# Kernel optimization log

Hardware: AMD Instinct MI355X
Metric: run time of the kernel (lower is better)

The kernel has to match this reference:

```python
import jax, jax.numpy as jnp
import numpy as np

N, E, G = 50000, 1600000, 64
IN, HID, OUT = 128, 64, 64
NEG_SLOPE = 0.2


def _p(key, shape):
    return jax.random.normal(key, shape, dtype=jnp.float32) * 0.1


def setup_inputs() -> dict:
    key = jax.random.key(0)
    ks = jax.random.split(key, 24)
    inp = {
        "x": jax.random.normal(ks[0], (N, IN), dtype=jnp.float32),
        "edge_index": jax.random.randint(ks[1], (2, E), 0, N),
        "edge_attr": jax.random.uniform(ks[2], (E, 1), dtype=jnp.float32),
        "batch": jnp.sort(jax.random.randint(ks[3], (N,), 0, G)),
        # GATv2 layer 1 (in=128 -> 64, heads=1)
        "Wl1": _p(ks[4], (IN, HID)), "bl1": _p(ks[5], (HID,)),
        "Wr1": _p(ks[6], (IN, HID)), "br1": _p(ks[7], (HID,)),
        "We1": _p(ks[8], (1, HID)), "att1": _p(ks[9], (HID,)), "bias1": _p(ks[10], (HID,)),
        # GATv2 layer 2 (64 -> 64)
        "Wl2": _p(ks[11], (HID, OUT)), "bl2": _p(ks[12], (OUT,)),
        "Wr2": _p(ks[13], (HID, OUT)), "br2": _p(ks[14], (OUT,)),
        "We2": _p(ks[15], (1, OUT)), "att2": _p(ks[16], (OUT,)), "bias2": _p(ks[17], (OUT,)),
        # MLP head: fc1 (64->32), bn1 (32), fc3 (32->1)
        "W_fc1": _p(ks[18], (OUT, OUT // 2)), "b_fc1": _p(ks[19], (OUT // 2,)),
        "bn_gamma": jnp.ones((OUT // 2,), jnp.float32),
        "bn_beta": jnp.zeros((OUT // 2,), jnp.float32),
        "bn_mean": _p(ks[20], (OUT // 2,)),
        "bn_var": jax.random.uniform(ks[21], (OUT // 2,), jnp.float32, 0.5, 1.5),
        "W_fc3": _p(ks[22], (OUT // 2, 1)), "b_fc3": _p(ks[23], (1,)),
    }
    return inp


def _add_self_loops(src, dst, edge_attr, n):
    # PyG add_self_loops with fill_value='mean': loop attr = mean of incoming edge attrs per node
    s = jax.ops.segment_sum(edge_attr, dst, num_segments=n)  # (N,1)
    c = jax.ops.segment_sum(jnp.ones((edge_attr.shape[0], 1), edge_attr.dtype), dst, num_segments=n)
    loop_attr = s / jnp.maximum(c, 1.0)
    loops = jnp.arange(n)
    return (jnp.concatenate([src, loops]), jnp.concatenate([dst, loops]),
            jnp.concatenate([edge_attr, loop_attr], axis=0))


def _gatv2(h, src, dst, e_attr, Wl, bl, Wr, br, We, att, bias, n):
    xl = h @ Wl + bl                     # (N, C) source transform
    xr = h @ Wr + br                     # (N, C) target transform
    ef = e_attr @ We                     # (E', C)
    s = jax.nn.leaky_relu(xl[src] + xr[dst] + ef, NEG_SLOPE)  # (E', C)
    logits = s @ att                     # (E',)
    m = jax.ops.segment_max(logits, dst, num_segments=n)
    m = jnp.where(jnp.isfinite(m), m, 0.0)
    p = jnp.exp(logits - m[dst])
    denom = jax.ops.segment_sum(p, dst, num_segments=n)
    alpha = p / (denom[dst] + 1e-16)
    out = jax.ops.segment_sum(alpha[:, None] * xl[src], dst, num_segments=n)
    return out + bias


def reference(x, edge_index, edge_attr, batch,
              Wl1, bl1, Wr1, br1, We1, att1, bias1,
              Wl2, bl2, Wr2, br2, We2, att2, bias2,
              W_fc1, b_fc1, bn_gamma, bn_beta, bn_mean, bn_var, W_fc3, b_fc3):
    n = x.shape[0]
    src, dst, ea = _add_self_loops(edge_index[0], edge_index[1], edge_attr, n)
    h = jax.nn.elu(_gatv2(x, src, dst, ea, Wl1, bl1, Wr1, br1, We1, att1, bias1, n))
    h = jax.nn.elu(_gatv2(h, src, dst, ea, Wl2, bl2, Wr2, br2, We2, att2, bias2, n))
    # global_mean_pool
    sums = jax.ops.segment_sum(h, batch, num_segments=G)
    cnts = jax.ops.segment_sum(jnp.ones((n, 1), h.dtype), batch, num_segments=G)
    pooled = sums / jnp.maximum(cnts, 1.0)
    # head: bn1(relu(fc1(.))) with eval-mode BN, dropout off, then fc3
    z = jax.nn.relu(pooled @ W_fc1 + b_fc1)
    z = (z - bn_mean) / jnp.sqrt(bn_var + 1e-5) * bn_gamma + bn_beta
    return z @ W_fc3 + b_fc3
```

## Files before the change

kernel.cpp:

```cpp
#include <hip/hip_runtime.h>
#include <hip/hip_fp16.h>
#include <math.h>

typedef unsigned long long u64;
typedef __attribute__((ext_vector_type(2))) _Float16 half2v;
typedef __attribute__((ext_vector_type(4))) _Float16 half4v;


#define CAP     3008
#define MAXSPAN 3072
#define PEPB    4096

__device__ __forceinline__ void xf_block(
        const float* __restrict__ h, int ld,
        const float* __restrict__ Wl, const float* __restrict__ bl,
        const float* __restrict__ Wr, const float* __restrict__ br,
        __half* __restrict__ xl, __half* __restrict__ xr,
        int N, int node0, _Float16* rows, int t) {
    int in_dim = 1 << ld;
    int q = in_dim >> 2;
    for (int idx = t; idx < 64 * q; idx += 256) {
        int nn = idx >> (ld - 2);
        int kk = (idx & (q - 1)) << 2;
        int node = node0 + nn;
        float4 v = {0.f, 0.f, 0.f, 0.f};
        if (node < N) v = *(const float4*)(h + (((size_t)node) << ld) + kk);
        half4v hv = {(_Float16)v.x, (_Float16)v.y, (_Float16)v.z, (_Float16)v.w};
        *(half4v*)(rows + (nn << ld) + kk) = hv;
    }
    __syncthreads();
    int lane = t & 63, w = t >> 6;
    int nb = w * 16;
    float al[16], ar[16];
    float blv = bl[lane], brv = br[lane];
#pragma unroll
    for (int i = 0; i < 16; ++i) { al[i] = blv; ar[i] = brv; }
    for (int k = 0; k < in_dim; k += 4) {
        float wl0 = Wl[(k + 0) * 64 + lane], wl1 = Wl[(k + 1) * 64 + lane];
        float wl2 = Wl[(k + 2) * 64 + lane], wl3 = Wl[(k + 3) * 64 + lane];
        float wr0 = Wr[(k + 0) * 64 + lane], wr1 = Wr[(k + 1) * 64 + lane];
        float wr2 = Wr[(k + 2) * 64 + lane], wr3 = Wr[(k + 3) * 64 + lane];
#pragma unroll
        for (int i = 0; i < 16; ++i) {
            half4v r = *(const half4v*)(rows + ((nb + i) << ld) + k);
            al[i] = fmaf((float)r.x, wl0, al[i]); al[i] = fmaf((float)r.y, wl1, al[i]);
            al[i] = fmaf((float)r.z, wl2, al[i]); al[i] = fmaf((float)r.w, wl3, al[i]);
            ar[i] = fmaf((float)r.x, wr0, ar[i]); ar[i] = fmaf((float)r.y, wr1, ar[i]);
            ar[i] = fmaf((float)r.z, wr2, ar[i]); ar[i] = fmaf((float)r.w, wr3, ar[i]);
        }
    }
#pragma unroll
    for (int i = 0; i < 16; ++i) {
        int node = node0 + nb + i;
        if (node < N) {
            xl[((size_t)node << 6) + lane] = __float2half(al[i]);
            xr[((size_t)node << 6) + lane] = __float2half(ar[i]);
        }
    }
}

union XfPartSmem {
    _Float16 rows[64 * 128];
    struct { int lh[800]; int lbase[800]; int lcur[800]; } p;
};

__global__ void k_xf1_part(
        const float* __restrict__ h, int ld,
        const float* __restrict__ Wl, const float* __restrict__ bl,
        const float* __restrict__ Wr, const float* __restrict__ br,
        __half* __restrict__ xl, __half* __restrict__ xr, int N, int nbXF,
        const int* __restrict__ ei, const float* __restrict__ ea,
        int* __restrict__ qtail, u64* __restrict__ queue, int E, int NB) {
    __shared__ XfPartSmem sm;
    int t = threadIdx.x;
    if (blockIdx.x < nbXF) {
        xf_block(h, ld, Wl, bl, Wr, br, xl, xr, N, blockIdx.x * 64, sm.rows, t);
    } else {
        int pb = blockIdx.x - nbXF;
        for (int i = t; i < NB; i += 256) { sm.p.lh[i] = 0; sm.p.lcur[i] = 0; }
        __syncthreads();
        int base = pb * PEPB;
        int end = base + PEPB; if (end > E) end = E;
        int dreg[PEPB / 256];
#pragma unroll
        for (int k = 0; k < PEPB / 256; ++k) {
            int e = base + t + k * 256;
            if (e < end) {
                dreg[k] = ei[E + e];
                atomicAdd(&sm.p.lh[dreg[k] >> 6], 1);
            }
        }
        __syncthreads();
        for (int i = t; i < NB; i += 256)
            if (sm.p.lh[i]) sm.p.lbase[i] = atomicAdd(&qtail[i], sm.p.lh[i]);
        __syncthreads();
#pragma unroll
        for (int k = 0; k < PEPB / 256; ++k) {
            int e = base + t + k * 256;
            if (e < end) {
                int d = dreg[k];
                int src = ei[e];
                float a = ea[e];
                int b = d >> 6;
                int idx = atomicAdd(&sm.p.lcur[b], 1);
                unsigned aq = (unsigned)(a * 16777216.0f);
                queue[(size_t)b * CAP + sm.p.lbase[b] + idx] =
                    (((u64)aq) << 24) | (((u64)(d & 63)) << 17) | (unsigned)src;
            }
        }
    }
}

__global__ void __launch_bounds__(1024)
k_bscan(const int* __restrict__ qtail, int* __restrict__ csrbase,
        int* __restrict__ row_start, int N, int NB,
        float* __restrict__ pooled, float* __restrict__ gcnt,
        int* __restrict__ done, int G) {
    __shared__ int s2[1024];
    int t = threadIdx.x;
    for (int i = t; i < G * 64; i += 1024) pooled[i] = 0.f;
    if (t < G) gcnt[t] = 0.f;
    if (t == 0) *done = 0;
    int lo = t << 6;
    int ndst = (lo < N) ? ((N - lo < 64) ? (N - lo) : 64) : 0;
    int cnt = (t < NB) ? qtail[t] : 0;
    int span = cnt + ndst;
    s2[t] = span;
    __syncthreads();
    for (int off = 1; off < 1024; off <<= 1) {
        int a = (t >= off) ? s2[t - off] : 0;
        __syncthreads();
        s2[t] += a;
        __syncthreads();
    }
    if (t < NB) csrbase[t] = s2[t] - span;
    if (t == 1023) {
        csrbase[NB] = s2[1023];
        row_start[N] = s2[1023];
    }
}

__device__ __forceinline__ unsigned attr_q15(float a) {
    unsigned short hb = __builtin_bit_cast(unsigned short, (_Float16)a);
    return (unsigned)(hb >> 1);
}

__global__ void k_build(const u64* __restrict__ queue, const int* __restrict__ qtail,
                        const int* __restrict__ csrbase,
                        int* __restrict__ row_start, unsigned* __restrict__ csr, int N) {
    __shared__ u64 stat[64];
    __shared__ int fill[64], sc[64];
    __shared__ unsigned lcsr[MAXSPAN];
    int t = threadIdx.x, b = blockIdx.x;
    if (t < 64) stat[t] = 0;
    __syncthreads();
    int cnt = qtail[b];
    size_t q0 = (size_t)b * CAP;
    for (int i = t; i < cnt; i += 256) {
        u64 r = queue[q0 + i];
        int dl = (int)((r >> 17) & 63);
        atomicAdd(&stat[dl], (1ULL << 32) | (unsigned)(r >> 24));
    }
    __syncthreads();
    int dg = (b << 6) + t;
    u64 p = (t < 64) ? stat[t] : 0;
    int deg = (int)(p >> 32);
    int v = (t < 64 && dg < N) ? deg + 1 : 0;
    if (t < 64) sc[t] = v;
    __syncthreads();
    for (int off = 1; off < 64; off <<= 1) {
        int a = (t >= off && t < 64) ? sc[t - off] : 0;
        __syncthreads();
        if (t < 64) sc[t] += a;
        __syncthreads();
    }
    if (t < 64 && dg < N) {
        int basel = sc[t] - v;
        row_start[dg] = csrbase[b] + basel;
        fill[t] = basel;
        float mean = ((float)(unsigned)p * (1.0f / 16777216.0f)) / fmaxf((float)deg, 1.0f);
        if (basel + deg < MAXSPAN) lcsr[basel + deg] = (attr_q15(mean) << 17) | (unsigned)dg;
    }
    __syncthreads();
    for (int i = t; i < cnt; i += 256) {
        u64 r = queue[q0 + i];
        int dl = (int)((r >> 17) & 63);
        int pos = atomicAdd(&fill[dl], 1);
        float av = (float)(unsigned)(r >> 24) * (1.0f / 16777216.0f);
        if (pos < MAXSPAN) lcsr[pos] = (attr_q15(av) << 17) | (unsigned)(r & 0x1FFFFu);
    }
    __syncthreads();
    int c0 = csrbase[b], span = csrbase[b + 1] - c0;
    if (span > MAXSPAN) span = MAXSPAN;
    for (int j = t; j < span; j += 256) csr[c0 + j] = lcsr[j];
}

__global__ void k_node_xf(const float* __restrict__ h, int ld,
                          const float* __restrict__ Wl, const float* __restrict__ bl,
                          const float* __restrict__ Wr, const float* __restrict__ br,
                          __half* __restrict__ xl, __half* __restrict__ xr, int N) {
    __shared__ _Float16 rows[64 * 64];
    xf_block(h, ld, Wl, bl, Wr, br, xl, xr, N, blockIdx.x * 64, rows, threadIdx.x);
}

#define EDGE_GROUP(r, xh, cc)                                                  \
    {                                                                          \
        _Float16 ah = __builtin_bit_cast(_Float16, (unsigned short)((r >> 16) & 0xFFFEu)); \
        half2v aa = {ah, ah};                                                  \
        half2v x01 = {xh.x, xh.y}, x23 = {xh.z, xh.w};                         \
        half2v v01 = aa * We01 + (x01 + xr01);                                 \
        half2v v23 = aa * We23 + (x23 + xr23);                                 \
        half2v s01 = __builtin_elementwise_max(v01, v01 * k02);                \
        half2v s23 = __builtin_elementwise_max(v23, v23 * k02);                \
        cc = __builtin_amdgcn_fdot2(s01, at01, 0.f, false);                    \
        cc = __builtin_amdgcn_fdot2(s23, at23, cc, false);                     \
    }

__global__ void k_attn(const __half* __restrict__ xl, const __half* __restrict__ xr,
                       const unsigned* __restrict__ csr, const int* __restrict__ row_start,
                       const float* __restrict__ We, const float* __restrict__ att,
                       const float* __restrict__ bias,
                       float* __restrict__ hout, int N) {
    int lane = threadIdx.x & 63;
    int d = (int)(((size_t)blockIdx.x * blockDim.x + threadIdx.x) >> 6);
    if (d >= N) return;
    int eq = lane >> 4;
    int fl = lane & 15;
    float4 Wef  = *(const float4*)(We + fl * 4);
    float4 attf = *(const float4*)(att + fl * 4);
    half2v We01 = {(_Float16)Wef.x, (_Float16)Wef.y};
    half2v We23 = {(_Float16)Wef.z, (_Float16)Wef.w};
    half2v at01 = {(_Float16)attf.x, (_Float16)attf.y};
    half2v at23 = {(_Float16)attf.z, (_Float16)attf.w};
    half4v xrh = *(const half4v*)(xr + ((size_t)d << 6) + fl * 4);
    half2v xr01 = {xrh.x, xrh.y}, xr23 = {xrh.z, xrh.w};
    const half2v k02 = {(_Float16)0.2f, (_Float16)0.2f};
    int e0 = __builtin_amdgcn_readfirstlane(row_start[d]);
    int e1 = __builtin_amdgcn_readfirstlane(row_start[d + 1]);
    float l = 0.f;
    float4 O = {0.f, 0.f, 0.f, 0.f};
    int e = e0;
    for (; e + 16 <= e1; e += 16) {
        unsigned rA = csr[e + eq];
        unsigned rB = csr[e + 4 + eq];
        unsigned rC = csr[e + 8 + eq];
        unsigned rD = csr[e + 12 + eq];
        half4v xA = *(const half4v*)(xl + (((size_t)(rA & 0x1FFFFu)) << 6) + fl * 4);
        half4v xB = *(const half4v*)(xl + (((size_t)(rB & 0x1FFFFu)) << 6) + fl * 4);
        half4v xC = *(const half4v*)(xl + (((size_t)(rC & 0x1FFFFu)) << 6) + fl * 4);
        half4v xD = *(const half4v*)(xl + (((size_t)(rD & 0x1FFFFu)) << 6) + fl * 4);
        float cA, cB, cC, cD;
        EDGE_GROUP(rA, xA, cA);
        EDGE_GROUP(rB, xB, cB);
        EDGE_GROUP(rC, xC, cC);
        EDGE_GROUP(rD, xD, cD);
#pragma unroll
        for (int mm = 1; mm <= 8; mm <<= 1) {
            cA += __shfl_xor(cA, mm, 64);
            cB += __shfl_xor(cB, mm, 64);
            cC += __shfl_xor(cC, mm, 64);
            cD += __shfl_xor(cD, mm, 64);
        }
        float qA = __expf(cA), qB = __expf(cB), qC = __expf(cC), qD = __expf(cD);
        l += (qA + qB) + (qC + qD);
        O.x = fmaf(qA, (float)xA.x, O.x); O.x = fmaf(qB, (float)xB.x, O.x);
        O.x = fmaf(qC, (float)xC.x, O.x); O.x = fmaf(qD, (float)xD.x, O.x);
        O.y = fmaf(qA, (float)xA.y, O.y); O.y = fmaf(qB, (float)xB.y, O.y);
        O.y = fmaf(qC, (float)xC.y, O.y); O.y = fmaf(qD, (float)xD.y, O.y);
        O.z = fmaf(qA, (float)xA.z, O.z); O.z = fmaf(qB, (float)xB.z, O.z);
        O.z = fmaf(qC, (float)xC.z, O.z); O.z = fmaf(qD, (float)xD.z, O.z);
        O.w = fmaf(qA, (float)xA.w, O.w); O.w = fmaf(qB, (float)xB.w, O.w);
        O.w = fmaf(qC, (float)xC.w, O.w); O.w = fmaf(qD, (float)xD.w, O.w);
    }
    for (; e < e1; e += 4) {
        int ee = e + eq;
        bool valid = ee < e1;
        unsigned r = csr[valid ? ee : (e1 - 1)];
        half4v xh = *(const half4v*)(xl + (((size_t)(r & 0x1FFFFu)) << 6) + fl * 4);
        float c;
        EDGE_GROUP(r, xh, c);
#pragma unroll
        for (int mm = 1; mm <= 8; mm <<= 1) c += __shfl_xor(c, mm, 64);
        float q = valid ? __expf(c) : 0.f;
        l += q;
        O.x = fmaf(q, (float)xh.x, O.x);
        O.y = fmaf(q, (float)xh.y, O.y);
        O.z = fmaf(q, (float)xh.z, O.z);
        O.w = fmaf(q, (float)xh.w, O.w);
    }
#pragma unroll
    for (int mm = 16; mm <= 32; mm <<= 1) {
        l   += __shfl_xor(l, mm, 64);
        O.x += __shfl_xor(O.x, mm, 64);
        O.y += __shfl_xor(O.y, mm, 64);
        O.z += __shfl_xor(O.z, mm, 64);
        O.w += __shfl_xor(O.w, mm, 64);
    }
    if (eq == 0) {
        float inv = 1.0f / (l + 1e-16f);
        float4 b4 = *(const float4*)(bias + fl * 4);
        float4 res;
        res.x = fmaf(O.x, inv, b4.x);
        res.y = fmaf(O.y, inv, b4.y);
        res.z = fmaf(O.z, inv, b4.z);
        res.w = fmaf(O.w, inv, b4.w);
        res.x = res.x > 0.f ? res.x : expm1f(res.x);
        res.y = res.y > 0.f ? res.y : expm1f(res.y);
        res.z = res.z > 0.f ? res.z : expm1f(res.z);
        res.w = res.w > 0.f ? res.w : expm1f(res.w);
        *(float4*)(hout + ((size_t)d << 6) + fl * 4) = res;
    }
}

__global__ void k_pool_head(const float* __restrict__ h, const int* __restrict__ batch,
                            float* __restrict__ pooled, float* __restrict__ gcnt,
                            int N, int npw, int* __restrict__ done,
                            const float* __restrict__ W1, const float* __restrict__ b1,
                            const float* __restrict__ gam, const float* __restrict__ bet,
                            const float* __restrict__ mu, const float* __restrict__ var,
                            const float* __restrict__ W3, const float* __restrict__ b3,
                            float* __restrict__ out, int G) {
    int tid = threadIdx.x;
    int lane = tid & 63;
    int wave = (int)(((size_t)blockIdx.x * blockDim.x + tid) >> 6);
    int begin = wave * npw;
    if (begin < N) {
        int end = begin + npw; if (end > N) end = N;
        int g = batch[begin];
        float acc = 0.f, cnt = 0.f;
        for (int n = begin; n < end; ++n) {
            int gn = batch[n];
            if (gn != g) {
                atomicAdd(&pooled[((size_t)g << 6) + lane], acc);
                if (lane == 0) atomicAdd(&gcnt[g], cnt);
                g = gn; acc = 0.f; cnt = 0.f;
            }
            acc += h[((size_t)n << 6) + lane];
            cnt += 1.f;
        }
        atomicAdd(&pooled[((size_t)g << 6) + lane], acc);
        if (lane == 0) atomicAdd(&gcnt[g], cnt);
    }
    __threadfence();
    __syncthreads();
    __shared__ int lastFlag;
    if (tid == 0) lastFlag = (atomicAdd(done, 1) == (int)gridDim.x - 1);
    __syncthreads();
    if (lastFlag && tid < G) {
        __threadfence();
        int g = tid;
        float inv = 1.0f / fmaxf(gcnt[g], 1.0f);
        float pr[64];
        for (int k = 0; k < 64; ++k) pr[k] = pooled[((size_t)g << 6) + k] * inv;
        float o = b3[0];
        for (int j = 0; j < 32; ++j) {
            float z = b1[j];
            for (int k = 0; k < 64; ++k) z += pr[k] * W1[k * 32 + j];
            z = fmaxf(z, 0.f);
            z = (z - mu[j]) / sqrtf(var[j] + 1e-5f) * gam[j] + bet[j];
            o += z * W3[j];
        }
        out[g] = o;
    }
}

extern "C" void kernel_launch(void* const* d_in, const int* in_sizes, int n_in,
                              void* d_out, int out_size, void* d_ws, size_t ws_size,
                              hipStream_t stream) {
    const float* x    = (const float*)d_in[0];
    const int*   ei   = (const int*)d_in[1];
    const float* ea   = (const float*)d_in[2];
    const int*   batch= (const int*)d_in[3];
    const float* Wl1  = (const float*)d_in[4];
    const float* bl1  = (const float*)d_in[5];
    const float* Wr1  = (const float*)d_in[6];
    const float* br1  = (const float*)d_in[7];
    const float* We1  = (const float*)d_in[8];
    const float* att1 = (const float*)d_in[9];
    const float* bi1  = (const float*)d_in[10];
    const float* Wl2  = (const float*)d_in[11];
    const float* bl2  = (const float*)d_in[12];
    const float* Wr2  = (const float*)d_in[13];
    const float* br2  = (const float*)d_in[14];
    const float* We2  = (const float*)d_in[15];
    const float* att2 = (const float*)d_in[16];
    const float* bi2  = (const float*)d_in[17];
    const float* Wf1  = (const float*)d_in[18];
    const float* bf1  = (const float*)d_in[19];
    const float* gam  = (const float*)d_in[20];
    const float* bet  = (const float*)d_in[21];
    const float* mu   = (const float*)d_in[22];
    const float* var  = (const float*)d_in[23];
    const float* Wf3  = (const float*)d_in[24];
    const float* bf3  = (const float*)d_in[25];

    const int N    = in_sizes[3];
    const int E    = in_sizes[2];
    const int INd  = in_sizes[0] / N;
    const int ld1  = (INd == 128) ? 7 : 6;
    const int Etot = E + N;
    const int G    = out_size;
    const int NB   = (N + 63) / 64;

    char* w = (char*)d_ws;
    auto carve = [&](size_t bytes) { char* p = w; w += (bytes + 255) & ~(size_t)255; return p; };
    __half*   xl       = (__half*)  carve((size_t)N * 64 * 2);
    __half*   xr       = (__half*)  carve((size_t)N * 64 * 2);
    float*    hbuf     = (float*)   carve((size_t)N * 64 * 4);
    unsigned* csr      = (unsigned*)carve((size_t)(Etot + 16) * 4);
    u64*      queue    = (u64*)     carve((size_t)NB * CAP * 8);
    int*      row_start= (int*)     carve((size_t)(N + 1) * 4);
    int*      qtail    = (int*)     carve((size_t)(NB + 1) * 4);
    int*      csrbase  = (int*)     carve((size_t)(NB + 1) * 4);
    float*    pooled   = (float*)   carve((size_t)G * 64 * 4);
    float*    gcnt     = (float*)   carve((size_t)G * 4);
    int*      done     = (int*)     carve(256);

    const int TB = 256;
    const int nbXF = (N + 63) / 64;
    const int attnBlocks = (N + 3) / 4;
    const int nbPart = (E + PEPB - 1) / PEPB;

    hipMemsetAsync(qtail, 0, (size_t)(NB + 1) * 4, stream);
    k_xf1_part<<<nbXF + nbPart, TB, 0, stream>>>(x, ld1, Wl1, bl1, Wr1, br1, xl, xr, N, nbXF,
                                                 ei, ea, qtail, queue, E, NB);
    k_bscan<<<1, 1024, 0, stream>>>(qtail, csrbase, row_start, N, NB,
                                    pooled, gcnt, done, G);
    k_build<<<NB, TB, 0, stream>>>(queue, qtail, csrbase, row_start, csr, N);

    k_attn<<<attnBlocks, TB, 0, stream>>>(xl, xr, csr, row_start, We1, att1, bi1, hbuf, N);

    k_node_xf<<<nbXF, TB, 0, stream>>>(hbuf, 6, Wl2, bl2, Wr2, br2, xl, xr, N);
    k_attn<<<attnBlocks, TB, 0, stream>>>(xl, xr, csr, row_start, We2, att2, bi2, hbuf, N);

    const int npw = 64;
    const int poolWaves = (N + npw - 1) / npw;
    k_pool_head<<<(poolWaves * 64 + TB - 1) / TB, TB, 0, stream>>>(
        hbuf, batch, pooled, gcnt, N, npw, done,
        Wf1, bf1, gam, bet, mu, var, Wf3, bf3, (float*)d_out, G);
}
```

Baseline: 358.1 us.

## Drop global bucket scan by using fixed-stride CSR slots per bucket

Removes the single-block prefix-scan kernel by giving each 64-node bucket a fixed MAXSPAN-sized CSR slot, with row ranges stored as packed (start,end) pairs per node. Pool accumulators are zeroed with a memset instead of inside the scan kernel. The partition kernel now processes 16384 edges per block with a strided loop rather than a register-held unrolled array. This saves one launch and one serialized scan, but makes the CSR buffer sparse and larger, and uses fewer, heavier partition blocks.

```diff
diff --git a/kernel.cpp b/kernel.cpp
--- a/kernel.cpp
+++ b/kernel.cpp
@@ -9,7 +9,7 @@
 
 #define CAP     3008
 #define MAXSPAN 3072
-#define PEPB    4096
+#define PEPB    16384
 
 __device__ __forceinline__ void xf_block(
         const float* __restrict__ h, int ld,
@@ -81,62 +81,24 @@
         __syncthreads();
         int base = pb * PEPB;
         int end = base + PEPB; if (end > E) end = E;
-        int dreg[PEPB / 256];
-#pragma unroll
-        for (int k = 0; k < PEPB / 256; ++k) {
-            int e = base + t + k * 256;
-            if (e < end) {
-                dreg[k] = ei[E + e];
-                atomicAdd(&sm.p.lh[dreg[k] >> 6], 1);
-            }
+        for (int e = base + t; e < end; e += 256) {
+            int d = ei[E + e];
+            atomicAdd(&sm.p.lh[d >> 6], 1);
         }
         __syncthreads();
         for (int i = t; i < NB; i += 256)
             if (sm.p.lh[i]) sm.p.lbase[i] = atomicAdd(&qtail[i], sm.p.lh[i]);
         __syncthreads();
-#pragma unroll
-        for (int k = 0; k < PEPB / 256; ++k) {
-            int e = base + t + k * 256;
-            if (e < end) {
-                int d = dreg[k];
-                int src = ei[e];
-                float a = ea[e];
-                int b = d >> 6;
-                int idx = atomicAdd(&sm.p.lcur[b], 1);
-                unsigned aq = (unsigned)(a * 16777216.0f);
-                queue[(size_t)b * CAP + sm.p.lbase[b] + idx] =
-                    (((u64)aq) << 24) | (((u64)(d & 63)) << 17) | (unsigned)src;
-            }
-        }
-    }
-}
-
-__global__ void __launch_bounds__(1024)
-k_bscan(const int* __restrict__ qtail, int* __restrict__ csrbase,
-        int* __restrict__ row_start, int N, int NB,
-        float* __restrict__ pooled, float* __restrict__ gcnt,
-        int* __restrict__ done, int G) {
-    __shared__ int s2[1024];
-    int t = threadIdx.x;
-    for (int i = t; i < G * 64; i += 1024) pooled[i] = 0.f;
-    if (t < G) gcnt[t] = 0.f;
-    if (t == 0) *done = 0;
-    int lo = t << 6;
-    int ndst = (lo < N) ? ((N - lo < 64) ? (N - lo) : 64) : 0;
-    int cnt = (t < NB) ? qtail[t] : 0;
-    int span = cnt + ndst;
-    s2[t] = span;
-    __syncthreads();
-    for (int off = 1; off < 1024; off <<= 1) {
-        int a = (t >= off) ? s2[t - off] : 0;
-        __syncthreads();
-        s2[t] += a;
-        __syncthreads();
-    }
-    if (t < NB) csrbase[t] = s2[t] - span;
-    if (t == 1023) {
-        csrbase[NB] = s2[1023];
-        row_start[N] = s2[1023];
+        for (int e = base + t; e < end; e += 256) {
+            int d = ei[E + e];
+            int src = ei[e];
+            float a = ea[e];
+            int b = d >> 6;
+            int idx = atomicAdd(&sm.p.lcur[b], 1);
+            unsigned aq = (unsigned)(a * 16777216.0f);
+            queue[(size_t)b * CAP + sm.p.lbase[b] + idx] =
+                (((u64)aq) << 24) | (((u64)(d & 63)) << 17) | (unsigned)src;
+        }
     }
 }
 
@@ -146,8 +108,7 @@
 }
 
 __global__ void k_build(const u64* __restrict__ queue, const int* __restrict__ qtail,
-                        const int* __restrict__ csrbase,
-                        int* __restrict__ row_start, unsigned* __restrict__ csr, int N) {
+                        u64* __restrict__ rs2, unsigned* __restrict__ csr, int N) {
     __shared__ u64 stat[64];
     __shared__ int fill[64], sc[64];
     __shared__ unsigned lcsr[MAXSPAN];
@@ -174,9 +135,10 @@
         if (t < 64) sc[t] += a;
         __syncthreads();
     }
+    int c0 = b * MAXSPAN;
     if (t < 64 && dg < N) {
         int basel = sc[t] - v;
-        row_start[dg] = csrbase[b] + basel;
+        rs2[dg] = (u64)(unsigned)(c0 + basel) | (((u64)(unsigned)(c0 + basel + deg + 1)) << 32);
         fill[t] = basel;
         float mean = ((float)(unsigned)p * (1.0f / 16777216.0f)) / fmaxf((float)deg, 1.0f);
         if (basel + deg < MAXSPAN) lcsr[basel + deg] = (attr_q15(mean) << 17) | (unsigned)dg;
@@ -190,7 +152,7 @@
         if (pos < MAXSPAN) lcsr[pos] = (attr_q15(av) << 17) | (unsigned)(r & 0x1FFFFu);
     }
     __syncthreads();
-    int c0 = csrbase[b], span = csrbase[b + 1] - c0;
+    int span = sc[63];
     if (span > MAXSPAN) span = MAXSPAN;
     for (int j = t; j < span; j += 256) csr[c0 + j] = lcsr[j];
 }
@@ -217,7 +179,7 @@
     }
 
 __global__ void k_attn(const __half* __restrict__ xl, const __half* __restrict__ xr,
-                       const unsigned* __restrict__ csr, const int* __restrict__ row_start,
+                       const unsigned* __restrict__ csr, const u64* __restrict__ rs2,
                        const float* __restrict__ We, const float* __restrict__ att,
                        const float* __restrict__ bias,
                        float* __restrict__ hout, int N) {
@@ -235,8 +197,9 @@
     half4v xrh = *(const half4v*)(xr + ((size_t)d << 6) + fl * 4);
     half2v xr01 = {xrh.x, xrh.y}, xr23 = {xrh.z, xrh.w};
     const half2v k02 = {(_Float16)0.2f, (_Float16)0.2f};
-    int e0 = __builtin_amdgcn_readfirstlane(row_start[d]);
-    int e1 = __builtin_amdgcn_readfirstlane(row_start[d + 1]);
+    u64 rr = rs2[d];
+    int e0 = __builtin_amdgcn_readfirstlane((int)(unsigned)rr);
+    int e1 = __builtin_amdgcn_readfirstlane((int)(unsigned)(rr >> 32));
     float l = 0.f;
     float4 O = {0.f, 0.f, 0.f, 0.f};
     int e = e0;
@@ -398,7 +361,6 @@
     const int E    = in_sizes[2];
     const int INd  = in_sizes[0] / N;
     const int ld1  = (INd == 128) ? 7 : 6;
-    const int Etot = E + N;
     const int G    = out_size;
     const int NB   = (N + 63) / 64;
 
@@ -407,11 +369,10 @@
     __half*   xl       = (__half*)  carve((size_t)N * 64 * 2);
     __half*   xr       = (__half*)  carve((size_t)N * 64 * 2);
     float*    hbuf     = (float*)   carve((size_t)N * 64 * 4);
-    unsigned* csr      = (unsigned*)carve((size_t)(Etot + 16) * 4);
+    unsigned* csr      = (unsigned*)carve((size_t)NB * MAXSPAN * 4);
     u64*      queue    = (u64*)     carve((size_t)NB * CAP * 8);
-    int*      row_start= (int*)     carve((size_t)(N + 1) * 4);
+    u64*      rs2      = (u64*)     carve((size_t)N * 8);
     int*      qtail    = (int*)     carve((size_t)(NB + 1) * 4);
-    int*      csrbase  = (int*)     carve((size_t)(NB + 1) * 4);
     float*    pooled   = (float*)   carve((size_t)G * 64 * 4);
     float*    gcnt     = (float*)   carve((size_t)G * 4);
     int*      done     = (int*)     carve(256);
@@ -422,16 +383,18 @@
     const int nbPart = (E + PEPB - 1) / PEPB;
 
     hipMemsetAsync(qtail, 0, (size_t)(NB + 1) * 4, stream);
+    size_t poolRegion = ((size_t)G * 64 * 4 + 255 & ~(size_t)255)
+                      + ((size_t)G * 4 + 255 & ~(size_t)255) + 256;
+    hipMemsetAsync(pooled, 0, poolRegion, stream);
+
     k_xf1_part<<<nbXF + nbPart, TB, 0, stream>>>(x, ld1, Wl1, bl1, Wr1, br1, xl, xr, N, nbXF,
                                                  ei, ea, qtail, queue, E, NB);
-    k_bscan<<<1, 1024, 0, stream>>>(qtail, csrbase, row_start, N, NB,
-                                    pooled, gcnt, done, G);
-    k_build<<<NB, TB, 0, stream>>>(queue, qtail, csrbase, row_start, csr, N);
-
-    k_attn<<<attnBlocks, TB, 0, stream>>>(xl, xr, csr, row_start, We1, att1, bi1, hbuf, N);
+    k_build<<<NB, TB, 0, stream>>>(queue, qtail, rs2, csr, N);
+
+    k_attn<<<attnBlocks, TB, 0, stream>>>(xl, xr, csr, rs2, We1, att1, bi1, hbuf, N);
 
     k_node_xf<<<nbXF, TB, 0, stream>>>(hbuf, 6, Wl2, bl2, Wr2, br2, xl, xr, N);
-    k_attn<<<attnBlocks, TB, 0, stream>>>(xl, xr, csr, row_start, We2, att2, bi2, hbuf, N);
+    k_attn<<<attnBlocks, TB, 0, stream>>>(xl, xr, csr, rs2, We2, att2, bi2, hbuf, N);
 
     const int npw = 64;
     const int poolWaves = (N + npw - 1) / npw;
```

New measurement: 368.3 us. 1.03x slower.
